# Performance work log

Measured on AMD Instinct MI355X. Metric: run time of the kernel, lower is better.

## Reference

```python
import jax, jax.numpy as jnp
import numpy as np

N_NODES = 20000
N_FEAT = 10
EDGE_DIM = 6
D = 256
H = 8
C = D // H  # 32 per-head channels for gat1/gat2
B = 2048
E = 320000
NEG = 0.2        # LeakyReLU slope in GATConv attention
BN_EPS = 1e-5


def _bn_eval(x, g, b):
    # BatchNorm1d in eval mode with fresh buffers: running_mean=0, running_var=1
    return g * x * (1.0 / np.sqrt(1.0 + BN_EPS)) + b


def _gat(x, src, dst, edge_attr, W, a_src, a_dst, We, a_e, bias, heads, out_ch, n):
    # PyG GATConv with edge_dim: shared src/dst linear, per-head additive attention
    xp = (x @ W).reshape(n, heads, out_ch)                       # [N,H,C]
    al_s = jnp.einsum('nhc,hc->nh', xp, a_src)                   # [N,H]
    al_d = jnp.einsum('nhc,hc->nh', xp, a_dst)                   # [N,H]
    ep = (edge_attr @ We).reshape(-1, heads, out_ch)             # [E,H,C]
    al_e = jnp.einsum('ehc,hc->eh', ep, a_e)                     # [E,H]
    alpha = jax.nn.leaky_relu(al_s[src] + al_d[dst] + al_e, NEG)  # [E,H]
    # segment softmax over incoming edges of each dst node
    amax = jax.ops.segment_max(alpha, dst, num_segments=n)
    amax = jnp.where(jnp.isfinite(amax), amax, 0.0)
    ex = jnp.exp(alpha - amax[dst])
    den = jax.ops.segment_sum(ex, dst, num_segments=n)
    w = ex / (den[dst] + 1e-16)
    out = jax.ops.segment_sum(xp[src] * w[..., None], dst, num_segments=n)
    return out.reshape(n, heads * out_ch) + bias


def setup_inputs():
    key = jax.random.key(0)
    ks = iter(jax.random.split(key, 40))
    def rn(shape, scale=0.05):
        return jax.random.normal(next(ks), shape, dtype=jnp.float32) * scale
    inp = {}
    inp['current_node_ids'] = jax.random.randint(next(ks), (B,), 0, N_NODES)
    inp['network_features'] = jax.random.normal(next(ks), (B, N_FEAT), dtype=jnp.float32)
    inp['edge_index'] = jax.random.randint(next(ks), (2, E), 0, N_NODES)
    inp['edge_attr'] = jax.random.normal(next(ks), (E, EDGE_DIM), dtype=jnp.float32)
    inp['emb'] = rn((N_NODES, D), 1.0)
    inp['net_w1'] = rn((N_FEAT, D)); inp['net_b1'] = jnp.zeros((D,), jnp.float32)
    inp['net_g1'] = jnp.ones((D,), jnp.float32); inp['net_be1'] = jnp.zeros((D,), jnp.float32)
    inp['net_w2'] = rn((D, D)); inp['net_b2'] = jnp.zeros((D,), jnp.float32)
    inp['net_g2'] = jnp.ones((D,), jnp.float32); inp['net_be2'] = jnp.zeros((D,), jnp.float32)
    for i, (h, c) in enumerate([(H, C), (H, C), (1, D)], start=1):
        inp[f'gat{i}_W'] = rn((D, h * c))
        inp[f'gat{i}_as'] = rn((h, c)); inp[f'gat{i}_ad'] = rn((h, c))
        inp[f'gat{i}_We'] = rn((EDGE_DIM, h * c)); inp[f'gat{i}_ae'] = rn((h, c))
        inp[f'gat{i}_b'] = jnp.zeros((h * c,), jnp.float32)
    inp['fus_w'] = rn((2 * D, D)); inp['fus_b'] = jnp.zeros((D,), jnp.float32)
    inp['fus_g'] = jnp.ones((D,), jnp.float32); inp['fus_be'] = jnp.zeros((D,), jnp.float32)
    inp['cls_w'] = rn((D, N_NODES)); inp['cls_b'] = jnp.zeros((N_NODES,), jnp.float32)
    return inp


def reference(current_node_ids, network_features, edge_index, edge_attr, emb,
              net_w1, net_b1, net_g1, net_be1, net_w2, net_b2, net_g2, net_be2,
              gat1_W, gat1_as, gat1_ad, gat1_We, gat1_ae, gat1_b,
              gat2_W, gat2_as, gat2_ad, gat2_We, gat2_ae, gat2_b,
              gat3_W, gat3_as, gat3_ad, gat3_We, gat3_ae, gat3_b,
              fus_w, fus_b, fus_g, fus_be, cls_w, cls_b):
    src, dst = edge_index[0], edge_index[1]
    n = emb.shape[0]
    x = jax.nn.relu(_gat(emb, src, dst, edge_attr, gat1_W, gat1_as, gat1_ad, gat1_We, gat1_ae, gat1_b, H, C, n))
    x = jax.nn.relu(_gat(x, src, dst, edge_attr, gat2_W, gat2_as, gat2_ad, gat2_We, gat2_ae, gat2_b, H, C, n))
    x = _gat(x, src, dst, edge_attr, gat3_W, gat3_as, gat3_ad, gat3_We, gat3_ae, gat3_b, 1, D, n)
    node_emb = x[current_node_ids]                               # [B,D]
    h1 = jax.nn.relu(_bn_eval(network_features @ net_w1 + net_b1, net_g1, net_be1))
    net_emb = jax.nn.relu(_bn_eval(h1 @ net_w2 + net_b2, net_g2, net_be2))
    combined = jnp.concatenate([node_emb, net_emb], axis=1)      # [B,2D]
    fused = jax.nn.relu(_bn_eval(combined @ fus_w + fus_b, fus_g, fus_be))
    return fused @ cls_w + cls_b                                 # [B, N_NODES]
```

## Files before the change

kernel.cpp:

```cpp
#include <hip/hip_runtime.h>

#define NEG_SLOPE 0.2f
static constexpr float BN_INV = 0.9999950000374997f;

typedef __bf16 bf16x8 __attribute__((ext_vector_type(8)));
typedef float  f32x4  __attribute__((ext_vector_type(4)));

__device__ inline float4 bf4f(ushort4 u){
  float4 r;
  r.x = __uint_as_float((unsigned)u.x << 16);
  r.y = __uint_as_float((unsigned)u.y << 16);
  r.z = __uint_as_float((unsigned)u.z << 16);
  r.w = __uint_as_float((unsigned)u.w << 16);
  return r;
}
__device__ inline ushort4 f4bf(float4 v){
  ushort4 u;
  u.x = __builtin_bit_cast(unsigned short, (__bf16)v.x);
  u.y = __builtin_bit_cast(unsigned short, (__bf16)v.y);
  u.z = __builtin_bit_cast(unsigned short, (__bf16)v.z);
  u.w = __builtin_bit_cast(unsigned short, (__bf16)v.w);
  return u;
}

__global__ void hist_kernel(const int* __restrict__ dst, int* __restrict__ cnt, int E){
  int e = blockIdx.x*256 + threadIdx.x;
  if (e < E) atomicAdd(&cnt[dst[e]], 1);
}

__global__ __launch_bounds__(1024) void scan1_kernel(int* __restrict__ cnt_cursor,
                                                     int* __restrict__ offs,
                                                     int* __restrict__ bsum, int n){
  __shared__ int wsum[16];
  int tid = threadIdx.x, lane = tid & 63, wv = tid >> 6;
  int i = blockIdx.x*1024 + tid;
  int v = (i < n) ? cnt_cursor[i] : 0;
  int x = v;
#pragma unroll
  for (int off = 1; off < 64; off <<= 1){
    int t = __shfl_up(x, off);
    if (lane >= off) x += t;
  }
  if (lane == 63) wsum[wv] = x;
  __syncthreads();
  int y = (lane < 16) ? wsum[lane] : 0;
#pragma unroll
  for (int off = 1; off < 16; off <<= 1){
    int t = __shfl_up(y, off);
    if (lane >= off) y += t;
  }
  int excl  = (wv == 0) ? 0 : __shfl(y, wv - 1);
  int total = __shfl(y, 15);
  int inc = excl + x;
  if (i < n){ offs[i+1] = inc; cnt_cursor[i] = inc - v; }
  if (tid == 0) bsum[blockIdx.x] = total;
}

__global__ void scan2_kernel(int* __restrict__ bsum, int nb){
  int lane = threadIdx.x;
  int v = (lane < nb) ? bsum[lane] : 0;
  int x = v;
#pragma unroll
  for (int off = 1; off < 64; off <<= 1){
    int t = __shfl_up(x, off);
    if (lane >= off) x += t;
  }
  if (lane < nb) bsum[lane] = x - v;
}

__global__ __launch_bounds__(1024) void scan3_kernel(int* __restrict__ offs, int* __restrict__ cursor,
                                                     const int* __restrict__ bsum, int n){
  int i = blockIdx.x*1024 + threadIdx.x;
  int base = bsum[blockIdx.x];
  if (i < n){ offs[i+1] += base; cursor[i] += base; }
  if (i == 0) offs[0] = 0;
}

__global__ void scatter_kernel(const int* __restrict__ src, const int* __restrict__ dst,
                               const float* __restrict__ ea, int* __restrict__ cursor,
                               int* __restrict__ perm_src, float* __restrict__ ea_perm, int E){
  int e = blockIdx.x*256 + threadIdx.x;
  if (e >= E) return;
  int d = dst[e];
  int pos = atomicAdd(&cursor[d], 1);
  perm_src[pos] = src[e];
#pragma unroll
  for (int k = 0; k < 6; ++k) ea_perm[(size_t)pos*6 + k] = ea[(size_t)e*6 + k];
}

template<bool USE_BIAS, bool USE_BN, bool USE_RELU, typename OutT>
__global__ __launch_bounds__(256) void gemm_kernel(
    const float* __restrict__ A, const float* __restrict__ W,
    const float* __restrict__ bias, const float* __restrict__ gam, const float* __restrict__ bet,
    OutT* __restrict__ C, int M, int N, int K, int LDC)
{
  __shared__ float As[32][68];
  __shared__ float Bs[32][64];
  int tid = threadIdx.x;
  int tx = tid & 15, ty = tid >> 4;
  int bn0 = blockIdx.x * 64, bm0 = blockIdx.y * 64;
  float acc[4][4] = {};
  for (int k0 = 0; k0 < K; k0 += 32){
    int kk = tid & 31, mm0 = tid >> 5;
#pragma unroll
    for (int r = 0; r < 8; ++r){
      int ml = mm0 + r*8;
      int m = bm0 + ml;
      As[kk][ml] = (m < M) ? A[(size_t)m*K + k0 + kk] : 0.f;
    }
    int nn = tid & 63, kb = tid >> 6;
#pragma unroll
    for (int r = 0; r < 8; ++r){
      int kl = kb + r*4;
      int n = bn0 + nn;
      Bs[kl][nn] = (n < N) ? W[(size_t)(k0 + kl)*N + n] : 0.f;
    }
    __syncthreads();
#pragma unroll
    for (int k = 0; k < 32; ++k){
      float4 a4 = *reinterpret_cast<const float4*>(&As[k][ty*4]);
      float4 b4 = *reinterpret_cast<const float4*>(&Bs[k][tx*4]);
      acc[0][0] += a4.x*b4.x; acc[0][1] += a4.x*b4.y; acc[0][2] += a4.x*b4.z; acc[0][3] += a4.x*b4.w;
      acc[1][0] += a4.y*b4.x; acc[1][1] += a4.y*b4.y; acc[1][2] += a4.y*b4.z; acc[1][3] += a4.y*b4.w;
      acc[2][0] += a4.z*b4.x; acc[2][1] += a4.z*b4.y; acc[2][2] += a4.z*b4.z; acc[2][3] += a4.z*b4.w;
      acc[3][0] += a4.w*b4.x; acc[3][1] += a4.w*b4.y; acc[3][2] += a4.w*b4.z; acc[3][3] += a4.w*b4.w;
    }
    __syncthreads();
  }
#pragma unroll
  for (int i = 0; i < 4; ++i){
    int m = bm0 + ty*4 + i;
    if (m < M){
#pragma unroll
      for (int j = 0; j < 4; ++j){
        int n = bn0 + tx*4 + j;
        if (n < N){
          float c = acc[i][j];
          if (USE_BIAS) c += bias[n];
          if (USE_BN)   c = gam[n]*c*BN_INV + bet[n];
          if (USE_RELU) c = fmaxf(c, 0.f);
          C[(size_t)m*LDC + n] = (OutT)c;
        }
      }
    }
  }
}

__global__ void wtrans_kernel(const float* __restrict__ W, __bf16* __restrict__ Wt, int K, int N){
  __shared__ float tile[32][33];
  int n0 = blockIdx.x*32, k0 = blockIdx.y*32;
  int t = threadIdx.x;
  int nl = t & 31, kl = t >> 5;
#pragma unroll
  for (int r = 0; r < 4; ++r)
    tile[kl + r*8][nl] = W[(size_t)(k0 + kl + r*8)*N + n0 + nl];
  __syncthreads();
  int nl2 = t >> 3, kc = (t & 7)*4;
#pragma unroll
  for (int j = 0; j < 4; ++j)
    Wt[(size_t)(n0 + nl2)*K + k0 + kc + j] = (__bf16)tile[kc + j][nl2];
}

__global__ void wtrans3_kernel(const float* __restrict__ W0, const float* __restrict__ W1,
                               const float* __restrict__ W2, __bf16* __restrict__ Wt,
                               const float* __restrict__ We1, const float* __restrict__ ae1,
                               const float* __restrict__ We2, const float* __restrict__ ae2,
                               const float* __restrict__ We3, const float* __restrict__ ae3,
                               float* __restrict__ M){
  if (blockIdx.z == 3){
    if (blockIdx.x != 0 || blockIdx.y != 0) return;
    int t = threadIdx.x;
    if (t < 96){
      const float* We = (t < 48) ? We1 : We2;
      const float* ae = (t < 48) ? ae1 : ae2;
      int u = t % 48, k = u / 8, h = u % 8;
      float s = 0.f;
      for (int c = 0; c < 32; ++c) s += We[k*256 + h*32 + c] * ae[h*32 + c];
      M[t] = s;
    } else if (t < 102){
      int k = t - 96;
      float s = 0.f;
      for (int c = 0; c < 256; ++c) s += We3[k*256 + c] * ae3[c];
      M[t] = s;
    }
    return;
  }
  __shared__ float tile[32][33];
  const float* W = (blockIdx.z == 0) ? W0 : (blockIdx.z == 1) ? W1 : W2;
  __bf16* D = Wt + (size_t)blockIdx.z * 65536;
  int n0 = blockIdx.x*32, k0 = blockIdx.y*32;
  int t = threadIdx.x;
  int nl = t & 31, kl = t >> 5;
#pragma unroll
  for (int r = 0; r < 4; ++r)
    tile[kl + r*8][nl] = W[(size_t)(k0 + kl + r*8)*256 + n0 + nl];
  __syncthreads();
  int nl2 = t >> 3, kc = (t & 7)*4;
#pragma unroll
  for (int j = 0; j < 4; ++j)
    D[(size_t)(n0 + nl2)*256 + k0 + kc + j] = (__bf16)tile[kc + j][nl2];
}

template<bool AF32, int ALSD, typename OutT>
__global__ __launch_bounds__(256) void mfma_gemm_kernel(
    const void* __restrict__ Aptr, const __bf16* __restrict__ Bt,
    OutT* __restrict__ C, int M, int N, int K,
    const float* __restrict__ a_s, const float* __restrict__ a_d,
    float* __restrict__ als, float* __restrict__ ald)
{
  const __bf16* Ab = (const __bf16*)Aptr;
  const float*  Af = (const float*) Aptr;
  __shared__ __bf16 As[128*72];
  __shared__ __bf16 Bs[128*72];
  int tid = threadIdx.x;
  int lane = tid & 63, w = tid >> 6;
  int quad = lane >> 4, l16 = lane & 15;
  int wm = (w & 1) * 64, wn = (w >> 1) * 64;
  int bn0 = blockIdx.x * 128, bm0 = blockIdx.y * 128;
  f32x4 acc[4][4] = {};
  for (int k0 = 0; k0 < K; k0 += 64){
#pragma unroll
    for (int p = 0; p < 4; ++p){
      int idx = p*256 + tid;
      int row = idx >> 3, ch = idx & 7;
      uint4 av;
      if constexpr (AF32){
        av = make_uint4(0,0,0,0);
        int m = bm0 + row;
        if (m < M){
          const float4* A4 = reinterpret_cast<const float4*>(&Af[(size_t)m*K + k0 + ch*8]);
          float4 x0 = A4[0], x1 = A4[1];
          ushort4 u0 = f4bf(x0), u1 = f4bf(x1);
          av = make_uint4((unsigned)u0.x | ((unsigned)u0.y << 16),
                          (unsigned)u0.z | ((unsigned)u0.w << 16),
                          (unsigned)u1.x | ((unsigned)u1.y << 16),
                          (unsigned)u1.z | ((unsigned)u1.w << 16));
        }
      } else {
        av = *reinterpret_cast<const uint4*>(&Ab[(size_t)(bm0 + row)*K + k0 + ch*8]);
      }
      *reinterpret_cast<uint4*>(&As[row*72 + ch*8]) = av;
      int n = bn0 + row;
      uint4 bv = make_uint4(0,0,0,0);
      if (n < N) bv = *reinterpret_cast<const uint4*>(&Bt[(size_t)n*K + k0 + ch*8]);
      *reinterpret_cast<uint4*>(&Bs[row*72 + ch*8]) = bv;
    }
    __syncthreads();
#pragma unroll
    for (int s = 0; s < 2; ++s){
      bf16x8 af[4], bfr[4];
#pragma unroll
      for (int t4 = 0; t4 < 4; ++t4){
        af[t4]  = *reinterpret_cast<const bf16x8*>(&As[(wm + t4*16 + l16)*72 + s*32 + quad*8]);
        bfr[t4] = *reinterpret_cast<const bf16x8*>(&Bs[(wn + t4*16 + l16)*72 + s*32 + quad*8]);
      }
#pragma unroll
      for (int mt = 0; mt < 4; ++mt)
#pragma unroll
        for (int nt = 0; nt < 4; ++nt)
          acc[mt][nt] = __builtin_amdgcn_mfma_f32_16x16x32_bf16(af[mt], bfr[nt], acc[mt][nt], 0, 0, 0);
    }
    __syncthreads();
  }
#pragma unroll
  for (int mt = 0; mt < 4; ++mt){
#pragma unroll
    for (int nt = 0; nt < 4; ++nt){
      int n = bn0 + wn + nt*16 + l16;
      if (n < N){
#pragma unroll
        for (int r = 0; r < 4; ++r){
          int m = bm0 + wm + mt*16 + quad*4 + r;
          if (m < M) C[(size_t)m*N + n] = (OutT)(acc[mt][nt][r]);
        }
      }
    }
  }
  if constexpr (ALSD != 0){
    float av4[4], dv4[4];
#pragma unroll
    for (int nt = 0; nt < 4; ++nt){
      int n = bn0 + wn + nt*16 + l16;
      av4[nt] = a_s[n];
      dv4[nt] = a_d[n];
    }
    int hb = (bn0 + wn) >> 5;
#pragma unroll
    for (int mt = 0; mt < 4; ++mt){
#pragma unroll
      for (int r = 0; r < 4; ++r){
        float s0 = acc[mt][0][r]*av4[0] + acc[mt][1][r]*av4[1];
        float s1 = acc[mt][2][r]*av4[2] + acc[mt][3][r]*av4[3];
        float d0 = acc[mt][0][r]*dv4[0] + acc[mt][1][r]*dv4[1];
        float d1 = acc[mt][2][r]*dv4[2] + acc[mt][3][r]*dv4[3];
#pragma unroll
        for (int off = 1; off < 16; off <<= 1){
          s0 += __shfl_xor(s0, off); s1 += __shfl_xor(s1, off);
          d0 += __shfl_xor(d0, off); d1 += __shfl_xor(d1, off);
        }
        if (l16 == 0){
          int m = bm0 + wm + mt*16 + quad*4 + r;
          if (m < M){
            if constexpr (ALSD == 8){
              als[m*8 + hb]     = s0; als[m*8 + hb + 1] = s1;
              ald[m*8 + hb]     = d0; ald[m*8 + hb + 1] = d1;
            } else {
              atomicAdd(&als[m], s0 + s1);
              atomicAdd(&ald[m], d0 + d1);
            }
          }
        }
      }
    }
  }
}

__global__ __launch_bounds__(512) void mfma_cls_kernel(
    const __bf16* __restrict__ A, const __bf16* __restrict__ Bt,
    const float* __restrict__ bias, float* __restrict__ C, int M, int N, int K)
{
  __shared__ __bf16 As[256*72];
  __shared__ __bf16 Bs[128*72];
  int tid = threadIdx.x;
  int lane = tid & 63, w = tid >> 6;
  int quad = lane >> 4, l16 = lane & 15;
  int wm = (w >> 1) * 64, wn = (w & 1) * 64;
  int nwg = gridDim.x;
  int chunk = nwg >> 3;
  int orig = (blockIdx.x & 7) * chunk + (blockIdx.x >> 3);
  int bm0 = (orig & 7) * 256, bn0 = (orig >> 3) * 128;
  f32x4 acc[4][4] = {};
  for (int k0 = 0; k0 < K; k0 += 64){
#pragma unroll
    for (int p = 0; p < 4; ++p){
      int idx = p*512 + tid;
      int row = idx >> 3, ch = idx & 7;
      uint4 av = *reinterpret_cast<const uint4*>(&A[(size_t)(bm0 + row)*K + k0 + ch*8]);
      *reinterpret_cast<uint4*>(&As[row*72 + ch*8]) = av;
    }
#pragma unroll
    for (int p = 0; p < 2; ++p){
      int idx = p*512 + tid;
      int row = idx >> 3, ch = idx & 7;
      int n = bn0 + row;
      uint4 bv = make_uint4(0,0,0,0);
      if (n < N) bv = *reinterpret_cast<const uint4*>(&Bt[(size_t)n*K + k0 + ch*8]);
      *reinterpret_cast<uint4*>(&Bs[row*72 + ch*8]) = bv;
    }
    __syncthreads();
#pragma unroll
    for (int s = 0; s < 2; ++s){
      bf16x8 af[4], bfr[4];
#pragma unroll
      for (int t4 = 0; t4 < 4; ++t4){
        af[t4]  = *reinterpret_cast<const bf16x8*>(&As[(wm + t4*16 + l16)*72 + s*32 + quad*8]);
        bfr[t4] = *reinterpret_cast<const bf16x8*>(&Bs[(wn + t4*16 + l16)*72 + s*32 + quad*8]);
      }
#pragma unroll
      for (int mt = 0; mt < 4; ++mt)
#pragma unroll
        for (int nt = 0; nt < 4; ++nt)
          acc[mt][nt] = __builtin_amdgcn_mfma_f32_16x16x32_bf16(af[mt], bfr[nt], acc[mt][nt], 0, 0, 0);
    }
    __syncthreads();
  }
#pragma unroll
  for (int mt = 0; mt < 4; ++mt){
#pragma unroll
    for (int nt = 0; nt < 4; ++nt){
      int n = bn0 + wn + nt*16 + l16;
      if (n < N){
        float bv = bias[n];
#pragma unroll
        for (int r = 0; r < 4; ++r){
          int m = bm0 + wm + mt*16 + quad*4 + r;
          C[(size_t)m*N + n] = acc[mt][nt][r] + bv;
        }
      }
    }
  }
}

__global__ void agg8_kernel(const int* __restrict__ offs, const int* __restrict__ perm_src,
                            const float* __restrict__ ea_perm, const float* __restrict__ Mf,
                            const float* __restrict__ als, const float* __restrict__ ald,
                            const __bf16* __restrict__ xp, const float* __restrict__ bias,
                            __bf16* __restrict__ out, int Nn){
  int gid = blockIdx.x*blockDim.x + threadIdx.x;
  int wave = gid >> 6, lane = threadIdx.x & 63;
  if (wave >= Nn) return;
  int beg = offs[wave], end = offs[wave+1];
  int hsel = lane >> 3;

  float mk[6];
#pragma unroll
  for (int k = 0; k < 6; ++k) mk[k] = Mf[k*8 + hsel];
  float aldv = ald[(size_t)wave*8 + hsel];

  const ushort4* X4 = reinterpret_cast<const ushort4*>(xp);
  float4 acc = make_float4(0.f,0.f,0.f,0.f);
  float den = 0.f;

  int i = beg;
  for (; i + 3 < end; i += 4){
    int s0 = perm_src[i], s1 = perm_src[i+1], s2 = perm_src[i+2], s3 = perm_src[i+3];
    float a0 = als[(size_t)s0*8 + hsel] + aldv;
    float a1 = als[(size_t)s1*8 + hsel] + aldv;
    float a2 = als[(size_t)s2*8 + hsel] + aldv;
    float a3 = als[(size_t)s3*8 + hsel] + aldv;
#pragma unroll
    for (int k = 0; k < 6; ++k){
      a0 += ea_perm[(size_t)i*6 + k]     * mk[k];
      a1 += ea_perm[(size_t)(i+1)*6 + k] * mk[k];
      a2 += ea_perm[(size_t)(i+2)*6 + k] * mk[k];
      a3 += ea_perm[(size_t)(i+3)*6 + k] * mk[k];
    }
    a0 = (a0 > 0.f) ? a0 : NEG_SLOPE*a0;
    a1 = (a1 > 0.f) ? a1 : NEG_SLOPE*a1;
    a2 = (a2 > 0.f) ? a2 : NEG_SLOPE*a2;
    a3 = (a3 > 0.f) ? a3 : NEG_SLOPE*a3;
    float e0 = __expf(a0), e1 = __expf(a1), e2 = __expf(a2), e3 = __expf(a3);
    den += (e0 + e1) + (e2 + e3);
    float4 x0 = bf4f(X4[(size_t)s0*64 + lane]);
    float4 x1 = bf4f(X4[(size_t)s1*64 + lane]);
    float4 x2 = bf4f(X4[(size_t)s2*64 + lane]);
    float4 x3 = bf4f(X4[(size_t)s3*64 + lane]);
    acc.x += x0.x*e0 + x1.x*e1 + x2.x*e2 + x3.x*e3;
    acc.y += x0.y*e0 + x1.y*e1 + x2.y*e2 + x3.y*e3;
    acc.z += x0.z*e0 + x1.z*e1 + x2.z*e2 + x3.z*e3;
    acc.w += x0.w*e0 + x1.w*e1 + x2.w*e2 + x3.w*e3;
  }
  for (; i < end; ++i){
    int s = perm_src[i];
    float a = als[(size_t)s*8 + hsel] + aldv;
#pragma unroll
    for (int k = 0; k < 6; ++k) a += ea_perm[(size_t)i*6 + k] * mk[k];
    a = (a > 0.f) ? a : NEG_SLOPE*a;
    float e = __expf(a);
    den += e;
    float4 xv = bf4f(X4[(size_t)s*64 + lane]);
    acc.x += xv.x*e; acc.y += xv.y*e; acc.z += xv.z*e; acc.w += xv.w*e;
  }

  float r = 1.f / (den + 1e-16f);
  float4 bv = reinterpret_cast<const float4*>(bias)[lane];
  acc.x = fmaxf(acc.x*r + bv.x, 0.f); acc.y = fmaxf(acc.y*r + bv.y, 0.f);
  acc.z = fmaxf(acc.z*r + bv.z, 0.f); acc.w = fmaxf(acc.w*r + bv.w, 0.f);
  reinterpret_cast<ushort4*>(out)[(size_t)wave*64 + lane] = f4bf(acc);
}

__global__ void agg1q_kernel(const int* __restrict__ ids, const int* __restrict__ offs,
                             const int* __restrict__ perm_src, const float* __restrict__ ea_perm,
                             const float* __restrict__ Mf, const float* __restrict__ als,
                             const float* __restrict__ ald, const __bf16* __restrict__ xp,
                             const float* __restrict__ bias, float* __restrict__ comb, int B){
  int gid = blockIdx.x*blockDim.x + threadIdx.x;
  int wave = gid >> 6, lane = threadIdx.x & 63;
  if (wave >= B) return;
  int node = ids[wave];
  int beg = offs[node], end = offs[node+1];

  float mk[6];
#pragma unroll
  for (int k = 0; k < 6; ++k) mk[k] = Mf[k];
  float aldv = ald[node];

  const ushort4* X4 = reinterpret_cast<const ushort4*>(xp);
  float4 acc = make_float4(0.f,0.f,0.f,0.f);
  float den = 0.f;

  int i = beg;
  for (; i + 3 < end; i += 4){
    int s0 = perm_src[i], s1 = perm_src[i+1], s2 = perm_src[i+2], s3 = perm_src[i+3];
    float a0 = als[s0] + aldv, a1 = als[s1] + aldv;
    float a2 = als[s2] + aldv, a3 = als[s3] + aldv;
#pragma unroll
    for (int k = 0; k < 6; ++k){
      a0 += ea_perm[(size_t)i*6 + k]     * mk[k];
      a1 += ea_perm[(size_t)(i+1)*6 + k] * mk[k];
      a2 += ea_perm[(size_t)(i+2)*6 + k] * mk[k];
      a3 += ea_perm[(size_t)(i+3)*6 + k] * mk[k];
    }
    a0 = (a0 > 0.f) ? a0 : NEG_SLOPE*a0;
    a1 = (a1 > 0.f) ? a1 : NEG_SLOPE*a1;
    a2 = (a2 > 0.f) ? a2 : NEG_SLOPE*a2;
    a3 = (a3 > 0.f) ? a3 : NEG_SLOPE*a3;
    float e0 = __expf(a0), e1 = __expf(a1), e2 = __expf(a2), e3 = __expf(a3);
    den += (e0 + e1) + (e2 + e3);
    float4 x0 = bf4f(X4[(size_t)s0*64 + lane]);
    float4 x1 = bf4f(X4[(size_t)s1*64 + lane]);
    float4 x2 = bf4f(X4[(size_t)s2*64 + lane]);
    float4 x3 = bf4f(X4[(size_t)s3*64 + lane]);
    acc.x += x0.x*e0 + x1.x*e1 + x2.x*e2 + x3.x*e3;
    acc.y += x0.y*e0 + x1.y*e1 + x2.y*e2 + x3.y*e3;
    acc.z += x0.z*e0 + x1.z*e1 + x2.z*e2 + x3.z*e3;
    acc.w += x0.w*e0 + x1.w*e1 + x2.w*e2 + x3.w*e3;
  }
  for (; i < end; ++i){
    int s = perm_src[i];
    float a = als[s] + aldv;
#pragma unroll
    for (int k = 0; k < 6; ++k) a += ea_perm[(size_t)i*6 + k] * mk[k];
    a = (a > 0.f) ? a : NEG_SLOPE*a;
    float e = __expf(a);
    den += e;
    float4 xv = bf4f(X4[(size_t)s*64 + lane]);
    acc.x += xv.x*e; acc.y += xv.y*e; acc.z += xv.z*e; acc.w += xv.w*e;
  }

  float r = 1.f / (den + 1e-16f);
  float4 bv = reinterpret_cast<const float4*>(bias)[lane];
  acc.x = acc.x*r + bv.x; acc.y = acc.y*r + bv.y;
  acc.z = acc.z*r + bv.z; acc.w = acc.w*r + bv.w;
  reinterpret_cast<float4*>(comb)[(size_t)wave*128 + lane] = acc;
}

__global__ void h1_kernel(const float* __restrict__ nf, const float* __restrict__ w1,
                          const float* __restrict__ b1, const float* __restrict__ g,
                          const float* __restrict__ be, float* __restrict__ out){
  int b = blockIdx.x, j = threadIdx.x;
  float s = b1[j];
#pragma unroll
  for (int k = 0; k < 10; ++k) s += nf[b*10 + k] * w1[k*256 + j];
  s = g[j]*s*BN_INV + be[j];
  out[b*256 + j] = fmaxf(s, 0.f);
}

extern "C" void kernel_launch(void* const* d_in, const int* in_sizes, int n_in,
                              void* d_out, int out_size, void* d_ws, size_t ws_size,
                              hipStream_t stream)
{
  const int*   ids   = (const int*)  d_in[0];
  const float* nf    = (const float*)d_in[1];
  const int*   eidx  = (const int*)  d_in[2];
  const float* eattr = (const float*)d_in[3];
  const float* emb   = (const float*)d_in[4];
  const float* w1    = (const float*)d_in[5];
  const float* b1    = (const float*)d_in[6];
  const float* g1    = (const float*)d_in[7];
  const float* be1   = (const float*)d_in[8];
  const float* w2    = (const float*)d_in[9];
  const float* b2    = (const float*)d_in[10];
  const float* g2    = (const float*)d_in[11];
  const float* be2   = (const float*)d_in[12];
  const float* gW[3]  = {(const float*)d_in[13], (const float*)d_in[19], (const float*)d_in[25]};
  const float* gas[3] = {(const float*)d_in[14], (const float*)d_in[20], (const float*)d_in[26]};
  const float* gad[3] = {(const float*)d_in[15], (const float*)d_in[21], (const float*)d_in[27]};
  const float* gWe[3] = {(const float*)d_in[16], (const float*)d_in[22], (const float*)d_in[28]};
  const float* gae[3] = {(const float*)d_in[17], (const float*)d_in[23], (const float*)d_in[29]};
  const float* gb[3]  = {(const float*)d_in[18], (const float*)d_in[24], (const float*)d_in[30]};
  const float* fus_w  = (const float*)d_in[31];
  const float* fus_b  = (const float*)d_in[32];
  const float* fus_g  = (const float*)d_in[33];
  const float* fus_be = (const float*)d_in[34];
  const float* cls_w  = (const float*)d_in[35];
  const float* cls_b  = (const float*)d_in[36];

  const int E  = in_sizes[3] / 6;
  const int Nn = in_sizes[4] / 256;
  const int B  = in_sizes[0];
  const int Ncls = in_sizes[36];
  const int Npad = (Nn + 127) & ~127;
  const int* src = eidx;
  const int* dst = eidx + E;

  char* wbase = (char*)d_ws;
  size_t woff = 0;
  auto carve = [&](size_t bytes)->void*{
    void* p = wbase + woff;
    woff = (woff + bytes + 255) & ~(size_t)255;
    return p;
  };
  int*    offs     = (int*)   carve((size_t)(Nn+1)*4);
  int*    cursor   = (int*)   carve((size_t)Nn*4);
  float*  als3     = (float*) carve((size_t)Nn*4);
  float*  ald3     = (float*) carve((size_t)Nn*4);
  size_t  zero_bytes = (size_t)((char*)ald3 - (char*)cursor) + (size_t)Nn*4;
  int*    bsum     = (int*)   carve(64*4);
  int*    perm_src = (int*)   carve((size_t)E*4);
  float*  ea_perm  = (float*) carve((size_t)E*6*4);
  __bf16* xb0      = (__bf16*)carve((size_t)Npad*256*2);
  __bf16* xb1      = (__bf16*)carve((size_t)Npad*256*2);
  __bf16* xpb      = (__bf16*)carve((size_t)Npad*256*2);
  __bf16* gWt      = (__bf16*)carve((size_t)3*256*256*2);
  float*  als      = (float*) carve((size_t)Nn*8*4);
  float*  ald      = (float*) carve((size_t)Nn*8*4);
  float*  Mfold    = (float*) carve(128*4);
  float*  h1b      = (float*) carve((size_t)B*256*4);
  float*  comb     = (float*) carve((size_t)B*512*4);
  __bf16* fusedb   = (__bf16*)carve((size_t)B*256*2);
  __bf16* clsWt    = (__bf16*)carve((size_t)Ncls*256*2);
  (void)ws_size; (void)n_in; (void)out_size;

  const int nb1024 = (Nn + 1023) / 1024;

  hipMemsetAsync(cursor, 0, zero_bytes, stream);
  hist_kernel<<<(E+255)/256, 256, 0, stream>>>(dst, cursor, E);
  scan1_kernel<<<nb1024, 1024, 0, stream>>>(cursor, offs, bsum, Nn);
  scan2_kernel<<<1, 64, 0, stream>>>(bsum, nb1024);
  scan3_kernel<<<nb1024, 1024, 0, stream>>>(offs, cursor, bsum, Nn);
  scatter_kernel<<<(E+255)/256, 256, 0, stream>>>(src, dst, eattr, cursor,
                                                  perm_src, ea_perm, E);

  wtrans3_kernel<<<dim3(8, 8, 4), 256, 0, stream>>>(gW[0], gW[1], gW[2], gWt,
                                                    gWe[0], gae[0], gWe[1], gae[1],
                                                    gWe[2], gae[2], Mfold);
  wtrans_kernel<<<dim3(Ncls/32, 256/32), 256, 0, stream>>>(cls_w, clsWt, 256, Ncls);

  dim3 mfma_grid_xp(2, Npad/128);
  int node_blocks = (Nn*64 + 255)/256;

  mfma_gemm_kernel<true, 8, __bf16><<<mfma_grid_xp, 256, 0, stream>>>(
      emb, gWt, xpb, Nn, 256, 256, gas[0], gad[0], als, ald);
  agg8_kernel<<<node_blocks, 256, 0, stream>>>(offs, perm_src, ea_perm, Mfold,
                                               als, ald, xpb, gb[0], xb1, Nn);
  mfma_gemm_kernel<false, 8, __bf16><<<mfma_grid_xp, 256, 0, stream>>>(
      xb1, gWt + 65536, xpb, Nn, 256, 256, gas[1], gad[1], als, ald);
  agg8_kernel<<<node_blocks, 256, 0, stream>>>(offs, perm_src, ea_perm, Mfold + 48,
                                               als, ald, xpb, gb[1], xb0, Nn);
  mfma_gemm_kernel<false, 1, __bf16><<<mfma_grid_xp, 256, 0, stream>>>(
      xb0, gWt + 131072, xpb, Nn, 256, 256, gas[2], gad[2], als3, ald3);
  agg1q_kernel<<<(B*64 + 255)/256, 256, 0, stream>>>(ids, offs, perm_src, ea_perm,
                                                     Mfold + 96, als3, ald3, xpb, gb[2], comb, B);

  h1_kernel<<<B, 256, 0, stream>>>(nf, w1, b1, g1, be1, h1b);
  gemm_kernel<true,true,true,float><<<dim3(4, B/64), 256, 0, stream>>>(
      h1b, w2, b2, g2, be2, comb + 256, B, 256, 256, 512);

  gemm_kernel<true,true,true,__bf16><<<dim3(4, B/64), 256, 0, stream>>>(
      comb, fus_w, fus_b, fus_g, fus_be, fusedb, B, 256, 512, 256);
  const int NB = (Ncls + 127) / 128;
  mfma_cls_kernel<<<8*NB, 512, 0, stream>>>(fusedb, clsWt, cls_b, (float*)d_out,
                                            B, Ncls, 256);
}
```

Before: 672.9 us.

## Fuse cls weight transpose into GEMM, merge scan2 into scan3, unroll agg8 by 8

The classifier GEMM now reads the fp32 cls_w directly, converting it to bf16 and transposing it into shared memory inside the kernel. This removes the separate wtrans kernel and its round trip through a bf16 copy. The scan2 block-prefix kernel is removed: each scan3 block sums the preceding block totals itself. The agg8 edge loop gains an 8-wide unrolled stage to expose more independent gathers. The costs are strided scalar bf16 stores into shared memory (possible bank conflicts) and the cls weight being reloaded as fp32 by each of the 8 M-tiles, which doubles those bytes.

```diff
diff --git a/kernel.cpp b/kernel.cpp
--- a/kernel.cpp
+++ b/kernel.cpp
@@ -56,22 +56,19 @@
   if (tid == 0) bsum[blockIdx.x] = total;
 }
 
-__global__ void scan2_kernel(int* __restrict__ bsum, int nb){
-  int lane = threadIdx.x;
-  int v = (lane < nb) ? bsum[lane] : 0;
-  int x = v;
-#pragma unroll
-  for (int off = 1; off < 64; off <<= 1){
-    int t = __shfl_up(x, off);
-    if (lane >= off) x += t;
-  }
-  if (lane < nb) bsum[lane] = x - v;
-}
-
 __global__ __launch_bounds__(1024) void scan3_kernel(int* __restrict__ offs, int* __restrict__ cursor,
                                                      const int* __restrict__ bsum, int n){
+  __shared__ int base_s;
+  if (threadIdx.x < 64){
+    int lane = threadIdx.x;
+    int v = (lane < (int)blockIdx.x) ? bsum[lane] : 0;
+#pragma unroll
+    for (int off = 1; off < 64; off <<= 1) v += __shfl_xor(v, off);
+    if (lane == 0) base_s = v;
+  }
+  __syncthreads();
+  int base = base_s;
   int i = blockIdx.x*1024 + threadIdx.x;
-  int base = bsum[blockIdx.x];
   if (i < n){ offs[i+1] += base; cursor[i] += base; }
   if (i == 0) offs[0] = 0;
 }
@@ -144,21 +141,6 @@
       }
     }
   }
-}
-
-__global__ void wtrans_kernel(const float* __restrict__ W, __bf16* __restrict__ Wt, int K, int N){
-  __shared__ float tile[32][33];
-  int n0 = blockIdx.x*32, k0 = blockIdx.y*32;
-  int t = threadIdx.x;
-  int nl = t & 31, kl = t >> 5;
-#pragma unroll
-  for (int r = 0; r < 4; ++r)
-    tile[kl + r*8][nl] = W[(size_t)(k0 + kl + r*8)*N + n0 + nl];
-  __syncthreads();
-  int nl2 = t >> 3, kc = (t & 7)*4;
-#pragma unroll
-  for (int j = 0; j < 4; ++j)
-    Wt[(size_t)(n0 + nl2)*K + k0 + kc + j] = (__bf16)tile[kc + j][nl2];
 }
 
 __global__ void wtrans3_kernel(const float* __restrict__ W0, const float* __restrict__ W1,
@@ -316,7 +298,7 @@
 }
 
 __global__ __launch_bounds__(512) void mfma_cls_kernel(
-    const __bf16* __restrict__ A, const __bf16* __restrict__ Bt,
+    const __bf16* __restrict__ A, const float* __restrict__ W,
     const float* __restrict__ bias, float* __restrict__ C, int M, int N, int K)
 {
   __shared__ __bf16 As[256*72];
@@ -329,6 +311,9 @@
   int chunk = nwg >> 3;
   int orig = (blockIdx.x & 7) * chunk + (blockIdx.x >> 3);
   int bm0 = (orig & 7) * 256, bn0 = (orig >> 3) * 128;
+  int kr = tid >> 5;
+  int nq = (tid & 31) * 4;
+  bool nok = (bn0 + nq) < N;
   f32x4 acc[4][4] = {};
   for (int k0 = 0; k0 < K; k0 += 64){
 #pragma unroll
@@ -339,13 +324,14 @@
       *reinterpret_cast<uint4*>(&As[row*72 + ch*8]) = av;
     }
 #pragma unroll
-    for (int p = 0; p < 2; ++p){
-      int idx = p*512 + tid;
-      int row = idx >> 3, ch = idx & 7;
-      int n = bn0 + row;
-      uint4 bv = make_uint4(0,0,0,0);
-      if (n < N) bv = *reinterpret_cast<const uint4*>(&Bt[(size_t)n*K + k0 + ch*8]);
-      *reinterpret_cast<uint4*>(&Bs[row*72 + ch*8]) = bv;
+    for (int p = 0; p < 4; ++p){
+      int kl = p*16 + kr;
+      float4 bv = make_float4(0.f,0.f,0.f,0.f);
+      if (nok) bv = *reinterpret_cast<const float4*>(&W[(size_t)(k0 + kl)*N + bn0 + nq]);
+      Bs[(nq+0)*72 + kl] = (__bf16)bv.x;
+      Bs[(nq+1)*72 + kl] = (__bf16)bv.y;
+      Bs[(nq+2)*72 + kl] = (__bf16)bv.z;
+      Bs[(nq+3)*72 + kl] = (__bf16)bv.w;
     }
     __syncthreads();
 #pragma unroll
@@ -402,6 +388,27 @@
   float den = 0.f;
 
   int i = beg;
+  for (; i + 7 < end; i += 8){
+    int ss[8];
+#pragma unroll
+    for (int u = 0; u < 8; ++u) ss[u] = perm_src[i+u];
+    float ee[8];
+#pragma unroll
+    for (int u = 0; u < 8; ++u){
+      float a = als[(size_t)ss[u]*8 + hsel] + aldv;
+#pragma unroll
+      for (int k = 0; k < 6; ++k) a += ea_perm[(size_t)(i+u)*6 + k] * mk[k];
+      a = (a > 0.f) ? a : NEG_SLOPE*a;
+      ee[u] = __expf(a);
+      den += ee[u];
+    }
+#pragma unroll
+    for (int u = 0; u < 8; ++u){
+      float4 xv = bf4f(X4[(size_t)ss[u]*64 + lane]);
+      acc.x += xv.x*ee[u]; acc.y += xv.y*ee[u];
+      acc.z += xv.z*ee[u]; acc.w += xv.w*ee[u];
+    }
+  }
   for (; i + 3 < end; i += 4){
     int s0 = perm_src[i], s1 = perm_src[i+1], s2 = perm_src[i+2], s3 = perm_src[i+3];
     float a0 = als[(size_t)s0*8 + hsel] + aldv;
@@ -589,7 +596,6 @@
   float*  h1b      = (float*) carve((size_t)B*256*4);
   float*  comb     = (float*) carve((size_t)B*512*4);
   __bf16* fusedb   = (__bf16*)carve((size_t)B*256*2);
-  __bf16* clsWt    = (__bf16*)carve((size_t)Ncls*256*2);
   (void)ws_size; (void)n_in; (void)out_size;
 
   const int nb1024 = (Nn + 1023) / 1024;
@@ -597,7 +603,6 @@
   hipMemsetAsync(cursor, 0, zero_bytes, stream);
   hist_kernel<<<(E+255)/256, 256, 0, stream>>>(dst, cursor, E);
   scan1_kernel<<<nb1024, 1024, 0, stream>>>(cursor, offs, bsum, Nn);
-  scan2_kernel<<<1, 64, 0, stream>>>(bsum, nb1024);
   scan3_kernel<<<nb1024, 1024, 0, stream>>>(offs, cursor, bsum, Nn);
   scatter_kernel<<<(E+255)/256, 256, 0, stream>>>(src, dst, eattr, cursor,
                                                   perm_src, ea_perm, E);
@@ -605,7 +610,6 @@
   wtrans3_kernel<<<dim3(8, 8, 4), 256, 0, stream>>>(gW[0], gW[1], gW[2], gWt,
                                                     gWe[0], gae[0], gWe[1], gae[1],
                                                     gWe[2], gae[2], Mfold);
-  wtrans_kernel<<<dim3(Ncls/32, 256/32), 256, 0, stream>>>(cls_w, clsWt, 256, Ncls);
 
   dim3 mfma_grid_xp(2, Npad/128);
   int node_blocks = (Nn*64 + 255)/256;
@@ -630,6 +634,6 @@
   gemm_kernel<true,true,true,__bf16><<<dim3(4, B/64), 256, 0, stream>>>(
       comb, fus_w, fus_b, fus_g, fus_be, fusedb, B, 256, 512, 256);
   const int NB = (Ncls + 127) / 128;
-  mfma_cls_kernel<<<8*NB, 512, 0, stream>>>(fusedb, clsWt, cls_b, (float*)d_out,
+  mfma_cls_kernel<<<8*NB, 512, 0, stream>>>(fusedb, cls_w, cls_b, (float*)d_out,
                                             B, Ncls, 256);
 }
```

Result: slower. 701.0 us (+4.2%).
